# Performance work log

Hardware: AMD Instinct MI355X
Metric: run time of the kernel (lower is better)

Reference implementation:

```python
import jax, jax.numpy as jnp
import numpy as np

N_NODES = 50000
N_EDGES = 600000
H_DIM = 128
N_RELS = 8
N_BASES = 4


def setup_inputs() -> dict:
    key = jax.random.key(0)
    ks = jax.random.split(key, 12)
    feats = jax.random.normal(ks[0], (N_NODES, H_DIM), dtype=jnp.float32)
    src = jax.random.randint(ks[1], (N_EDGES,), 0, N_NODES, dtype=jnp.int64)
    dst = jax.random.randint(ks[2], (N_EDGES,), 0, N_NODES, dtype=jnp.int64)
    etype = jax.random.randint(ks[3], (N_EDGES,), 0, N_RELS, dtype=jnp.int64)
    norm = jax.random.uniform(ks[4], (N_EDGES, 1), dtype=jnp.float32)
    s = 1.0 / np.sqrt(H_DIM)
    # layer 0 params (basis decomposition: W_r = sum_b comp[r,b] * basis[b])
    basis0 = jax.random.normal(ks[5], (N_BASES, H_DIM, H_DIM), dtype=jnp.float32) * s
    comp0 = jax.random.normal(ks[6], (N_RELS, N_BASES), dtype=jnp.float32)
    bias0 = jnp.zeros((H_DIM,), dtype=jnp.float32)
    # layer 1 params
    basis1 = jax.random.normal(ks[7], (N_BASES, H_DIM, H_DIM), dtype=jnp.float32) * s
    comp1 = jax.random.normal(ks[8], (N_RELS, N_BASES), dtype=jnp.float32)
    bias1 = jnp.zeros((H_DIM,), dtype=jnp.float32)
    return {"feats": feats, "src": src, "dst": dst, "etype": etype, "norm": norm,
            "basis0": basis0, "comp0": comp0, "bias0": bias0,
            "basis1": basis1, "comp1": comp1, "bias1": bias1}


def _rel_graph_conv(h, src, dst, etype, norm, basis, comp, bias):
    # basis-decomposed relation weights: [R, d_in, d_out]
    W = jnp.einsum('rb,bdo->rdo', comp, basis)
    # transform all nodes under every relation: [R, N, d_out]
    Hr = jnp.einsum('nd,rdo->rno', h, W)
    # gather per-edge message by (relation, source node), apply edge norm
    msg = Hr[etype, src] * norm  # [E, d_out]
    # scatter-sum into destination nodes
    agg = jax.ops.segment_sum(msg, dst, num_segments=h.shape[0])
    return jax.nn.relu(agg + bias)


def reference(feats, src, dst, etype, norm, basis0, comp0, bias0, basis1, comp1, bias1):
    h = _rel_graph_conv(feats, src, dst, etype, norm, basis0, comp0, bias0)
    h = _rel_graph_conv(h, src, dst, etype, norm, basis1, comp1, bias1)
    return h
```

## Files before the change

kernel.cpp:

```cpp
#include <hip/hip_runtime.h>

#define H    128
#define NB   4
#define DT   32

typedef __attribute__((ext_vector_type(8))) short short8;
typedef __attribute__((ext_vector_type(4))) float f32x4;

static __device__ __forceinline__ unsigned short f2bf(float f) {
    unsigned u = __float_as_uint(f);
    unsigned r = (u + 0x7fffu + ((u >> 16) & 1u)) >> 16;
    return (unsigned short)r;
}
static __device__ __forceinline__ float bfe(short s) {
    return __uint_as_float(((unsigned)(unsigned short)s) << 16);
}

__global__ __launch_bounds__(256) void hist_rank(const int* __restrict__ dst,
                                                 int* __restrict__ counts,
                                                 int* __restrict__ rank, int E) {
    int e = blockIdx.x * 256 + threadIdx.x;
    if (e < E) rank[e] = atomicAdd(&counts[dst[e]], 1);
}

__global__ __launch_bounds__(1024) void scan_blocks(const int* __restrict__ counts,
                                                    int* __restrict__ partial,
                                                    int* __restrict__ blocksums, int n) {
    __shared__ int buf[1024];
    int tid = threadIdx.x;
    int i = blockIdx.x * 1024 + tid;
    buf[tid] = (i < n) ? counts[i] : 0;
    __syncthreads();
#pragma unroll
    for (int off = 1; off < 1024; off <<= 1) {
        int t = (tid >= off) ? buf[tid - off] : 0;
        __syncthreads();
        buf[tid] += t;
        __syncthreads();
    }
    if (i < n) partial[i] = buf[tid];
    if (tid == 1023) blocksums[blockIdx.x] = buf[1023];
}

__global__ __launch_bounds__(64) void scan_carry(int* __restrict__ blocksums, int nb) {
    int tid = threadIdx.x;
    int v = (tid < nb) ? blocksums[tid] : 0;
#pragma unroll
    for (int off = 1; off < 64; off <<= 1) {
        int t = __shfl_up(v, off);
        if (tid >= off) v += t;
    }
    if (tid < nb) blocksums[tid] = v;
}

__global__ __launch_bounds__(256) void scan_add(const int* __restrict__ partial,
                                                const int* __restrict__ blocksums,
                                                int* __restrict__ offs, int n) {
    int i = blockIdx.x * 256 + threadIdx.x;
    if (i >= n) return;
    int b = i >> 10;
    int carry = (b > 0) ? blocksums[b - 1] : 0;
    offs[i + 1] = partial[i] + carry;
    if (i == 0) offs[0] = 0;
}

__global__ __launch_bounds__(256) void scatter_edges(
        const int* __restrict__ src, const int* __restrict__ dst,
        const int* __restrict__ etype, const float* __restrict__ norm,
        const int* __restrict__ offs, const int* __restrict__ rank,
        uint2* __restrict__ er, int E) {
    int e = blockIdx.x * 256 + threadIdx.x;
    if (e >= E) return;
    int pos = offs[dst[e]] + rank[e];
    uint2 r;
    r.x = (unsigned)src[e] | ((unsigned)etype[e] << 17);
    r.y = __float_as_uint(norm[e]);
    er[pos] = r;
}

__global__ __launch_bounds__(256) void convert_bf16(const float* __restrict__ in,
                                                    unsigned short* __restrict__ out, int n4) {
    int i = blockIdx.x * 256 + threadIdx.x;
    if (i >= n4) return;
    float4 v = ((const float4*)in)[i];
    ushort4 o;
    o.x = f2bf(v.x); o.y = f2bf(v.y); o.z = f2bf(v.z); o.w = f2bf(v.w);
    ((ushort4*)out)[i] = o;
}

__global__ __launch_bounds__(128) void make_wb(
        const float* __restrict__ basis0, const float* __restrict__ basis1,
        unsigned short* __restrict__ Wb) {
    int b = blockIdx.x;
    int d = blockIdx.y;
    int l = blockIdx.z;
    int o = threadIdx.x;
    const float* basis = l ? basis1 : basis0;
    float s = basis[((size_t)b * H + d) * H + o];
    Wb[((size_t)l * H + o) * (NB * H) + b * H + d] = f2bf(s);
}

#define EACC(R, HV) {                                                   \
    const float* cp = cmp + ((R.x >> 17) & 7) * 4;                      \
    float w = __uint_as_float(R.y);                                     \
    float wa = w * cp[0], wb = w * cp[1];                               \
    float wc = w * cp[2], wd = w * cp[3];                               \
    _Pragma("unroll")                                                   \
    for (int c = 0; c < 8; ++c) {                                       \
        float f = bfe(HV[c]);                                           \
        a0[c] = fmaf(wa, f, a0[c]); a1[c] = fmaf(wb, f, a1[c]);         \
        a2[c] = fmaf(wc, f, a2[c]); a3[c] = fmaf(wd, f, a3[c]);         \
    } }

__global__ __launch_bounds__(512, 4) void fused_layer(
        const unsigned short* __restrict__ hin,
        const int* __restrict__ offs,
        const uint2* __restrict__ er,
        const float* __restrict__ comp,
        const unsigned short* __restrict__ Wb,
        const float* __restrict__ bias,
        void* __restrict__ outp, int M, int write_bf16) {
    __shared__ char lds[DT * 1024];
    __shared__ float cmp[32];
    const int tid  = threadIdx.x;
    if (tid < 32) cmp[tid] = comp[tid];
    __syncthreads();

    const int nl   = tid >> 4;
    const int ch   = tid & 15;
    const int v0   = blockIdx.x * DT;
    const int v    = v0 + nl;

    float a0[8], a1[8], a2[8], a3[8];
#pragma unroll
    for (int c = 0; c < 8; ++c) { a0[c] = 0.f; a1[c] = 0.f; a2[c] = 0.f; a3[c] = 0.f; }

    if (v < M) {
        const int beg = offs[v], end = offs[v + 1];
        int e = beg;
        for (; e + 4 <= end; e += 4) {
            uint2 r0 = er[e];
            uint2 r1 = er[e + 1];
            uint2 r2 = er[e + 2];
            uint2 r3 = er[e + 3];
            short8 h0 = *(const short8*)(hin + (size_t)(r0.x & 0x1FFFF) * H + ch * 8);
            short8 h1 = *(const short8*)(hin + (size_t)(r1.x & 0x1FFFF) * H + ch * 8);
            short8 h2 = *(const short8*)(hin + (size_t)(r2.x & 0x1FFFF) * H + ch * 8);
            short8 h3 = *(const short8*)(hin + (size_t)(r3.x & 0x1FFFF) * H + ch * 8);
            EACC(r0, h0) EACC(r1, h1) EACC(r2, h2) EACC(r3, h3)
        }
        for (; e < end; ++e) {
            uint2 r0 = er[e];
            short8 h0 = *(const short8*)(hin + (size_t)(r0.x & 0x1FFFF) * H + ch * 8);
            EACC(r0, h0)
        }
    }

    {
        char* row = lds + nl * 1024;
        const int swz = (nl & 7) << 4;
        uint4 pk;
#define PACK(A) pk.x = (unsigned)f2bf(A[0]) | ((unsigned)f2bf(A[1]) << 16); \
                pk.y = (unsigned)f2bf(A[2]) | ((unsigned)f2bf(A[3]) << 16); \
                pk.z = (unsigned)f2bf(A[4]) | ((unsigned)f2bf(A[5]) << 16); \
                pk.w = (unsigned)f2bf(A[6]) | ((unsigned)f2bf(A[7]) << 16);
        PACK(a0) *(uint4*)(row + ((0 * 256 + ch * 16) ^ swz)) = pk;
        PACK(a1) *(uint4*)(row + ((1 * 256 + ch * 16) ^ swz)) = pk;
        PACK(a2) *(uint4*)(row + ((2 * 256 + ch * 16) ^ swz)) = pk;
        PACK(a3) *(uint4*)(row + ((3 * 256 + ch * 16) ^ swz)) = pk;
#undef PACK
    }
    __syncthreads();

    const int wid  = tid >> 6;
    const int lane = tid & 63;
    const int n0 = wid * 16;
    const int lr = lane & 15;
    const int lg = lane >> 4;
    const char* bbase = (const char*)Wb + (size_t)(n0 + lr) * (NB * H) * 2;
    const int swz = (lr & 7) << 4;

    f32x4 acc0 = (f32x4){0.f, 0.f, 0.f, 0.f};
    f32x4 acc1 = (f32x4){0.f, 0.f, 0.f, 0.f};
#pragma unroll
    for (int ks = 0; ks < 16; ++ks) {
        const int kb = ks * 64 + lg * 16;
        short8 b   = *(const short8*)(bbase + kb);
        short8 av0 = *(const short8*)(lds + (lr)      * 1024 + (kb ^ swz));
        short8 av1 = *(const short8*)(lds + (16 + lr) * 1024 + (kb ^ swz));
        acc0 = __builtin_amdgcn_mfma_f32_16x16x32_bf16(av0, b, acc0, 0, 0, 0);
        acc1 = __builtin_amdgcn_mfma_f32_16x16x32_bf16(av1, b, acc1, 0, 0, 0);
    }

    const float bcol = bias[n0 + lr];
#pragma unroll
    for (int m = 0; m < 2; ++m) {
        const f32x4 a = m ? acc1 : acc0;
#pragma unroll
        for (int j = 0; j < 4; ++j) {
            const int rl   = m * 16 + lg * 4 + j;
            const int grow = v0 + rl;
            if (grow < M) {
                float val = fmaxf(a[j] + bcol, 0.f);
                if (write_bf16)
                    ((unsigned short*)outp)[(size_t)grow * H + n0 + lr] = f2bf(val);
                else
                    ((float*)outp)[(size_t)grow * H + n0 + lr] = val;
            }
        }
    }
}

extern "C" void kernel_launch(void* const* d_in, const int* in_sizes, int n_in,
                              void* d_out, int out_size, void* d_ws, size_t ws_size,
                              hipStream_t stream) {
    const float* feats  = (const float*)d_in[0];
    const int*   src    = (const int*)  d_in[1];
    const int*   dst    = (const int*)  d_in[2];
    const int*   etype  = (const int*)  d_in[3];
    const float* norm   = (const float*)d_in[4];
    const float* basis0 = (const float*)d_in[5];
    const float* comp0  = (const float*)d_in[6];
    const float* bias0  = (const float*)d_in[7];
    const float* basis1 = (const float*)d_in[8];
    const float* comp1  = (const float*)d_in[9];
    const float* bias1  = (const float*)d_in[10];
    float* out = (float*)d_out;

    const int M = in_sizes[0] / H;
    const int E = in_sizes[1];

    char* ws = (char*)d_ws;
    size_t cur = 0;
    auto take = [&](size_t bytes) { void* p = ws + cur; cur += (bytes + 255) & ~(size_t)255; return p; };
    unsigned short* hbf  = (unsigned short*)take((size_t)M * H * 2);
    unsigned short* h1bf = (unsigned short*)take((size_t)M * H * 2);
    unsigned short* Wb   = (unsigned short*)take((size_t)2 * H * NB * H * 2);
    int*   counts  = (int*)take((size_t)M * 4);
    int*   offs    = (int*)take((size_t)(M + 1) * 4);
    int*   partial = (int*)take((size_t)M * 4);
    int*   bsums   = (int*)take((size_t)64 * 4);
    int*   rank    = (int*)take((size_t)E * 4);
    uint2* er      = (uint2*)take((size_t)E * 8);

    dim3 blk(256);
    int eb  = (E + 255) / 256;
    int n4  = M * H / 4;
    int cb  = (n4 + 255) / 256;
    int mb  = (M + 255) / 256;
    int nsb = (M + 1023) / 1024;
    int fb  = (M + DT - 1) / DT;

    hipMemsetAsync(counts, 0, (size_t)M * 4, stream);
    hist_rank    <<<eb, blk, 0, stream>>>(dst, counts, rank, E);
    scan_blocks  <<<nsb, 1024, 0, stream>>>(counts, partial, bsums, M);
    scan_carry   <<<1, 64, 0, stream>>>(bsums, nsb);
    scan_add     <<<mb, blk, 0, stream>>>(partial, bsums, offs, M);
    scatter_edges<<<eb, blk, 0, stream>>>(src, dst, etype, norm, offs, rank, er, E);
    convert_bf16 <<<cb, blk, 0, stream>>>(feats, hbf, n4);
    make_wb      <<<dim3(NB, H, 2), 128, 0, stream>>>(basis0, basis1, Wb);

    fused_layer<<<fb, 512, 0, stream>>>(hbf, offs, er, comp0, Wb, bias0, h1bf, M, 1);
    fused_layer<<<fb, 512, 0, stream>>>(h1bf, offs, er, comp1,
                                        Wb + (size_t)H * NB * H, bias1, out, M, 0);
}
```

Baseline: 194.6 us.

## Sort nodes by in-degree and shrink fused layer blocks to 16 nodes

Adds a degree-histogram counting sort that orders destination nodes by descending in-degree, and the fused layer reads nodes through this permutation so the nodes sharing a block have similar edge counts. Blocks drop from 32 nodes and 512 threads to 16 nodes and 256 threads. Each wave now computes 32 output columns for 16 rows instead of 16 columns for 32 rows, and the edge loop unrolls by 2 instead of 4. This targets load imbalance between nodes of different degree, at the cost of three extra small kernels, scattered output writes, and less overlap of gather loads per thread.

```diff
diff --git a/kernel.cpp b/kernel.cpp
--- a/kernel.cpp
+++ b/kernel.cpp
@@ -2,7 +2,7 @@
 
 #define H    128
 #define NB   4
-#define DT   32
+#define NPB  16
 
 typedef __attribute__((ext_vector_type(8))) short short8;
 typedef __attribute__((ext_vector_type(4))) float f32x4;
@@ -62,6 +62,33 @@
     int carry = (b > 0) ? blocksums[b - 1] : 0;
     offs[i + 1] = partial[i] + carry;
     if (i == 0) offs[0] = 0;
+}
+
+__global__ __launch_bounds__(256) void deg_hist(const int* __restrict__ counts,
+                                                int* __restrict__ dbin, int M) {
+    int v = blockIdx.x * 256 + threadIdx.x;
+    if (v < M) atomicAdd(&dbin[63 - min(counts[v], 63)], 1);
+}
+
+__global__ __launch_bounds__(64) void deg_scan(int* __restrict__ dbin) {
+    int tid = threadIdx.x;
+    int v = dbin[tid];
+    int inc = v;
+#pragma unroll
+    for (int off = 1; off < 64; off <<= 1) {
+        int t = __shfl_up(inc, off);
+        if (tid >= off) inc += t;
+    }
+    dbin[tid] = inc - v;
+}
+
+__global__ __launch_bounds__(256) void deg_scatter(const int* __restrict__ counts,
+                                                   int* __restrict__ dbin,
+                                                   int* __restrict__ perm, int M) {
+    int v = blockIdx.x * 256 + threadIdx.x;
+    if (v >= M) return;
+    int pos = atomicAdd(&dbin[63 - min(counts[v], 63)], 1);
+    perm[pos] = v;
 }
 
 __global__ __launch_bounds__(256) void scatter_edges(
@@ -112,44 +139,44 @@
         a2[c] = fmaf(wc, f, a2[c]); a3[c] = fmaf(wd, f, a3[c]);         \
     } }
 
-__global__ __launch_bounds__(512, 4) void fused_layer(
+__global__ __launch_bounds__(256, 8) void fused_layer(
         const unsigned short* __restrict__ hin,
         const int* __restrict__ offs,
         const uint2* __restrict__ er,
+        const int* __restrict__ perm,
         const float* __restrict__ comp,
         const unsigned short* __restrict__ Wb,
         const float* __restrict__ bias,
         void* __restrict__ outp, int M, int write_bf16) {
-    __shared__ char lds[DT * 1024];
+    __shared__ char lds[NPB * 1024];
     __shared__ float cmp[32];
-    const int tid  = threadIdx.x;
+    __shared__ int   gvs[NPB];
+    const int tid = threadIdx.x;
     if (tid < 32) cmp[tid] = comp[tid];
     __syncthreads();
 
-    const int nl   = tid >> 4;
-    const int ch   = tid & 15;
-    const int v0   = blockIdx.x * DT;
-    const int v    = v0 + nl;
+    const int nl = tid >> 4;
+    const int ch = tid & 15;
+    const int v0 = blockIdx.x * NPB;
+    const int v  = (v0 + nl < M) ? perm[v0 + nl] : -1;
+    if (ch == 0) gvs[nl] = v;
 
     float a0[8], a1[8], a2[8], a3[8];
 #pragma unroll
     for (int c = 0; c < 8; ++c) { a0[c] = 0.f; a1[c] = 0.f; a2[c] = 0.f; a3[c] = 0.f; }
 
-    if (v < M) {
+    if (v >= 0) {
         const int beg = offs[v], end = offs[v + 1];
         int e = beg;
-        for (; e + 4 <= end; e += 4) {
+        for (; e + 2 <= end; e += 2) {
             uint2 r0 = er[e];
             uint2 r1 = er[e + 1];
-            uint2 r2 = er[e + 2];
-            uint2 r3 = er[e + 3];
             short8 h0 = *(const short8*)(hin + (size_t)(r0.x & 0x1FFFF) * H + ch * 8);
             short8 h1 = *(const short8*)(hin + (size_t)(r1.x & 0x1FFFF) * H + ch * 8);
-            short8 h2 = *(const short8*)(hin + (size_t)(r2.x & 0x1FFFF) * H + ch * 8);
-            short8 h3 = *(const short8*)(hin + (size_t)(r3.x & 0x1FFFF) * H + ch * 8);
-            EACC(r0, h0) EACC(r1, h1) EACC(r2, h2) EACC(r3, h3)
+            EACC(r0, h0)
+            EACC(r1, h1)
         }
-        for (; e < end; ++e) {
+        if (e < end) {
             uint2 r0 = er[e];
             short8 h0 = *(const short8*)(hin + (size_t)(r0.x & 0x1FFFF) * H + ch * 8);
             EACC(r0, h0)
@@ -174,10 +201,12 @@
 
     const int wid  = tid >> 6;
     const int lane = tid & 63;
-    const int n0 = wid * 16;
     const int lr = lane & 15;
     const int lg = lane >> 4;
-    const char* bbase = (const char*)Wb + (size_t)(n0 + lr) * (NB * H) * 2;
+    const int n0 = wid * 16;
+    const char* b0base = (const char*)Wb + (size_t)(n0 + lr) * (NB * H) * 2;
+    const char* b1base = (const char*)Wb + (size_t)(n0 + 64 + lr) * (NB * H) * 2;
+    const char* abase  = lds + lr * 1024;
     const int swz = (lr & 7) << 4;
 
     f32x4 acc0 = (f32x4){0.f, 0.f, 0.f, 0.f};
@@ -185,27 +214,30 @@
 #pragma unroll
     for (int ks = 0; ks < 16; ++ks) {
         const int kb = ks * 64 + lg * 16;
-        short8 b   = *(const short8*)(bbase + kb);
-        short8 av0 = *(const short8*)(lds + (lr)      * 1024 + (kb ^ swz));
-        short8 av1 = *(const short8*)(lds + (16 + lr) * 1024 + (kb ^ swz));
-        acc0 = __builtin_amdgcn_mfma_f32_16x16x32_bf16(av0, b, acc0, 0, 0, 0);
-        acc1 = __builtin_amdgcn_mfma_f32_16x16x32_bf16(av1, b, acc1, 0, 0, 0);
-    }
-
-    const float bcol = bias[n0 + lr];
-#pragma unroll
-    for (int m = 0; m < 2; ++m) {
-        const f32x4 a = m ? acc1 : acc0;
+        short8 a  = *(const short8*)(abase + (kb ^ swz));
+        short8 b0 = *(const short8*)(b0base + kb);
+        short8 b1 = *(const short8*)(b1base + kb);
+        acc0 = __builtin_amdgcn_mfma_f32_16x16x32_bf16(a, b0, acc0, 0, 0, 0);
+        acc1 = __builtin_amdgcn_mfma_f32_16x16x32_bf16(a, b1, acc1, 0, 0, 0);
+    }
+
+    const float bc0 = bias[n0 + lr];
+    const float bc1 = bias[n0 + 64 + lr];
+#pragma unroll
+    for (int g = 0; g < 2; ++g) {
+        const f32x4 a = g ? acc1 : acc0;
+        const int col = n0 + g * 64 + lr;
+        const float bc = g ? bc1 : bc0;
 #pragma unroll
         for (int j = 0; j < 4; ++j) {
-            const int rl   = m * 16 + lg * 4 + j;
-            const int grow = v0 + rl;
-            if (grow < M) {
-                float val = fmaxf(a[j] + bcol, 0.f);
+            const int rl = lg * 4 + j;
+            const int grow = gvs[rl];
+            if (grow >= 0) {
+                float val = fmaxf(a[j] + bc, 0.f);
                 if (write_bf16)
-                    ((unsigned short*)outp)[(size_t)grow * H + n0 + lr] = f2bf(val);
+                    ((unsigned short*)outp)[(size_t)grow * H + col] = f2bf(val);
                 else
-                    ((float*)outp)[(size_t)grow * H + n0 + lr] = val;
+                    ((float*)outp)[(size_t)grow * H + col] = val;
             }
         }
     }
@@ -240,6 +272,8 @@
     int*   offs    = (int*)take((size_t)(M + 1) * 4);
     int*   partial = (int*)take((size_t)M * 4);
     int*   bsums   = (int*)take((size_t)64 * 4);
+    int*   perm    = (int*)take((size_t)M * 4);
+    int*   dbin    = (int*)take((size_t)64 * 4);
     int*   rank    = (int*)take((size_t)E * 4);
     uint2* er      = (uint2*)take((size_t)E * 8);
 
@@ -249,10 +283,14 @@
     int cb  = (n4 + 255) / 256;
     int mb  = (M + 255) / 256;
     int nsb = (M + 1023) / 1024;
-    int fb  = (M + DT - 1) / DT;
+    int fb  = (M + NPB - 1) / NPB;
 
     hipMemsetAsync(counts, 0, (size_t)M * 4, stream);
+    hipMemsetAsync(dbin, 0, 64 * 4, stream);
     hist_rank    <<<eb, blk, 0, stream>>>(dst, counts, rank, E);
+    deg_hist     <<<mb, blk, 0, stream>>>(counts, dbin, M);
+    deg_scan     <<<1, 64, 0, stream>>>(dbin);
+    deg_scatter  <<<mb, blk, 0, stream>>>(counts, dbin, perm, M);
     scan_blocks  <<<nsb, 1024, 0, stream>>>(counts, partial, bsums, M);
     scan_carry   <<<1, 64, 0, stream>>>(bsums, nsb);
     scan_add     <<<mb, blk, 0, stream>>>(partial, bsums, offs, M);
@@ -260,7 +298,7 @@
     convert_bf16 <<<cb, blk, 0, stream>>>(feats, hbf, n4);
     make_wb      <<<dim3(NB, H, 2), 128, 0, stream>>>(basis0, basis1, Wb);
 
-    fused_layer<<<fb, 512, 0, stream>>>(hbf, offs, er, comp0, Wb, bias0, h1bf, M, 1);
-    fused_layer<<<fb, 512, 0, stream>>>(h1bf, offs, er, comp1,
+    fused_layer<<<fb, blk, 0, stream>>>(hbf, offs, er, perm, comp0, Wb, bias0, h1bf, M, 1);
+    fused_layer<<<fb, blk, 0, stream>>>(h1bf, offs, er, perm, comp1,
                                         Wb + (size_t)H * NB * H, bias1, out, M, 0);
 }
```

After: 629.4 us. 3.23x slower.
